# Performance work log

Hardware: AMD Instinct MI355X
Metric: run time of the kernel (lower is better)

## Reference

```python
import jax, jax.numpy as jnp
import numpy as np

N = 1048576   # total points across batch
C = 64        # in_planes
B = 16        # number of ragged segments (point clouds)
EPS = 1e-5


def setup_inputs() -> dict:
    key = jax.random.key(0)
    ks = jax.random.split(key, 4)
    x = jax.random.normal(ks[0], (N, C), dtype=jnp.float32)
    # cumulative end-offsets, strictly increasing, last == N
    rng = np.random.default_rng(0)
    w = rng.random(B) + 0.5
    ends = np.round(np.cumsum(w) / w.sum() * N).astype(np.int64)
    ends[-1] = N
    o = jnp.asarray(ends)
    # linear2: Linear(C, C) + ReLU (applied to per-segment mean)
    W2 = jax.random.normal(ks[1], (C, C), dtype=jnp.float32) / np.float32(np.sqrt(C))
    b2 = jnp.zeros((C,), jnp.float32)
    # linear1: BasicMLP(2C -> C): Linear + norm + ReLU
    W1 = jax.random.normal(ks[2], (2 * C, C), dtype=jnp.float32) / np.float32(np.sqrt(2 * C))
    b1 = jnp.zeros((C,), jnp.float32)
    gamma = jnp.ones((C,), jnp.float32)
    beta = jnp.zeros((C,), jnp.float32)
    return dict(x=x, o=o, W2=W2, b2=b2, W1=W1, b1=b1, gamma=gamma, beta=beta)


def reference(x, o, W2, b2, W1, b1, gamma, beta):
    n = x.shape[0]
    nseg = o.shape[0]
    # segment id of each point from cumulative offsets o
    seg = jnp.searchsorted(o, jnp.arange(n), side='right')          # [N]
    counts = jnp.diff(o, prepend=0).astype(x.dtype)                 # [B]
    # per-segment mean pool (x_b.sum(0) / cnt)
    sums = jax.ops.segment_sum(x, seg, num_segments=nseg)           # [B, C]
    means = sums / counts[:, None]
    # linear2: Linear + ReLU on the pooled vector
    xb = jax.nn.relu(means @ W2 + b2)                               # [B, C]
    # broadcast-repeat pooled feature back to points, concat with x
    h = jnp.concatenate([x, xb[seg]], axis=1)                       # [N, 2C]
    # linear1: Linear -> norm (LayerNorm stand-in for conditional norm) -> ReLU
    h = h @ W1 + b1                                                 # [N, C]
    mu = jnp.mean(h, axis=-1, keepdims=True)
    var = jnp.var(h, axis=-1, keepdims=True)
    h = (h - mu) * jax.lax.rsqrt(var + EPS) * gamma + beta
    return jax.nn.relu(h)
```

## Files before the change

kernel.cpp:

```cpp
#include <hip/hip_runtime.h>
#include <hip/hip_bf16.h>
#include <cstddef>

constexpr int C = 64;
constexpr int B = 16;

typedef __attribute__((ext_vector_type(8))) short bf16x8;
typedef __attribute__((ext_vector_type(4))) float f32x4;
typedef __attribute__((ext_vector_type(4))) unsigned int u32x4;

__device__ inline unsigned short f2bf(float f) {
    unsigned u = __builtin_bit_cast(unsigned, f);
    unsigned r = (u + 0x7FFFu + ((u >> 16) & 1u)) >> 16;
    return (unsigned short)r;
}

__device__ inline unsigned pk2(float a, float b) {
    __hip_bfloat162 t = __float22bfloat162_rn(float2{a, b});
    unsigned u;
    __builtin_memcpy(&u, &t, 4);
    return u;
}

__device__ inline bf16x8 cvt8(float4 u, float4 v) {
    u32x4 r;
    r[0] = pk2(u.x, u.y);
    r[1] = pk2(u.z, u.w);
    r[2] = pk2(v.x, v.y);
    r[3] = pk2(v.z, v.w);
    return __builtin_bit_cast(bf16x8, r);
}

__global__ __launch_bounds__(256) void seg_sum_kernel(
    const float* __restrict__ x, const int* __restrict__ o,
    float* __restrict__ sums, int N, int rows_per_block)
{
    __shared__ float lsum[B * C];
    const int tid = threadIdx.x;
    for (int i = tid; i < B * C; i += 256) lsum[i] = 0.0f;
    __syncthreads();

    const int c4 = (tid & 15) * 4;
    const int r0 = tid >> 4;
    const int row_begin = blockIdx.x * rows_per_block;
    const int row_end   = min(N, row_begin + rows_per_block);

    float ax = 0.f, ay = 0.f, az = 0.f, aw = 0.f;
    int seg = 0;
    int endcur = o[0];

    for (int r = row_begin + r0; r < row_end; r += 16) {
        while (r >= endcur) {
            if (ax != 0.f || ay != 0.f || az != 0.f || aw != 0.f) {
                atomicAdd(&lsum[seg * C + c4 + 0], ax);
                atomicAdd(&lsum[seg * C + c4 + 1], ay);
                atomicAdd(&lsum[seg * C + c4 + 2], az);
                atomicAdd(&lsum[seg * C + c4 + 3], aw);
                ax = ay = az = aw = 0.f;
            }
            ++seg;
            endcur = o[seg];
        }
        const float4 v = *reinterpret_cast<const float4*>(x + (size_t)r * C + c4);
        ax += v.x; ay += v.y; az += v.z; aw += v.w;
    }
    if (ax != 0.f || ay != 0.f || az != 0.f || aw != 0.f) {
        atomicAdd(&lsum[seg * C + c4 + 0], ax);
        atomicAdd(&lsum[seg * C + c4 + 1], ay);
        atomicAdd(&lsum[seg * C + c4 + 2], az);
        atomicAdd(&lsum[seg * C + c4 + 3], aw);
    }
    __syncthreads();

    for (int i = tid; i < B * C; i += 256) {
        const float v = lsum[i];
        if (v != 0.f) atomicAdd(&sums[i], v);
    }
}

__global__ __launch_bounds__(256) void main_mfma_kernel(
    const float* __restrict__ x, const int* __restrict__ o,
    const float* __restrict__ sums,
    const float* __restrict__ W2, const float* __restrict__ b2,
    const float* __restrict__ W1, const float* __restrict__ b1,
    const float* __restrict__ gamma, const float* __restrict__ beta,
    float* __restrict__ out, int N, int rows_per_wave)
{
    __shared__ float ms[B * C];
    __shared__ float xbs[B * C];
    __shared__ float vl[B * C];
    __shared__ unsigned short wbfs[4096];
    __shared__ int osh[B];

    const int tid = threadIdx.x;
    if (tid < B) osh[tid] = o[tid];
    __syncthreads();

    const int j = tid & 63;
    const int bq = tid >> 6;

#pragma unroll
    for (int q = 0; q < 4; ++q) {
        const int b = bq * 4 + q;
        const int cnt = osh[b] - (b ? osh[b - 1] : 0);
        ms[b * C + j] = sums[b * C + j] / (float)cnt;
    }
    __syncthreads();

    {
        float acc[4];
        const float bj = b2[j];
#pragma unroll
        for (int q = 0; q < 4; ++q) acc[q] = bj;
        for (int c = 0; c < C; ++c) {
            const float wv = W2[c * C + j];
#pragma unroll
            for (int q = 0; q < 4; ++q)
                acc[q] = fmaf(ms[(bq * 4 + q) * C + c], wv, acc[q]);
        }
#pragma unroll
        for (int q = 0; q < 4; ++q) xbs[(bq * 4 + q) * C + j] = fmaxf(acc[q], 0.f);
    }
    __syncthreads();

    {
        float acc[4];
        const float bj = b1[j];
#pragma unroll
        for (int q = 0; q < 4; ++q) acc[q] = bj;
        for (int jj = 0; jj < C; ++jj) {
            const float wv = W1[(C + jj) * C + j];
#pragma unroll
            for (int q = 0; q < 4; ++q)
                acc[q] = fmaf(xbs[(bq * 4 + q) * C + jj], wv, acc[q]);
        }
#pragma unroll
        for (int q = 0; q < 4; ++q) vl[(bq * 4 + q) * C + j] = acc[q];
    }

    for (int idx = tid; idx < 4096; idx += 256) {
        const int jj2 = idx & 7;
        const int ln  = (idx >> 3) & 63;
        const int tt  = (idx >> 9) & 1;
        const int ct  = idx >> 10;
        const int k   = tt * 32 + ((ln >> 4) * 8) + jj2;
        const int ch  = 4 * (ln & 15) + ct;
        wbfs[idx] = f2bf(W1[k * C + ch]);
    }
    __syncthreads();

    const int lane = tid & 63;
    const int wid  = tid >> 6;
    const int chb  = lane & 15;
    const int prow = (lane >> 4) * 4;

    bf16x8 wf[4][2];
#pragma unroll
    for (int ct = 0; ct < 4; ++ct)
#pragma unroll
        for (int t = 0; t < 2; ++t)
            wf[ct][t] = *reinterpret_cast<const bf16x8*>(wbfs + ((ct * 2 + t) * 64 + lane) * 8);

    const float4 g4  = *reinterpret_cast<const float4*>(gamma + 4 * chb);
    const float4 bt4 = *reinterpret_cast<const float4*>(beta  + 4 * chb);

    const int gw = blockIdx.x * 4 + wid;
    const int p_begin = gw * rows_per_wave;
    if (p_begin >= N) return;
    const int p_end = min(N, p_begin + rows_per_wave);

    int seg = 0;
    while (p_begin >= osh[seg]) ++seg;
    float4 vb = *reinterpret_cast<const float4*>(vl + seg * C + 4 * chb);

    for (int p0 = p_begin; p0 < p_end; p0 += 16) {
        const float* xr = x + (size_t)(p0 + chb) * C + ((lane >> 4) * 8);
        const float4 a0 = *reinterpret_cast<const float4*>(xr);
        const float4 a1 = *reinterpret_cast<const float4*>(xr + 4);
        const float4 a2 = *reinterpret_cast<const float4*>(xr + 32);
        const float4 a3 = *reinterpret_cast<const float4*>(xr + 36);
        const bf16x8 A0 = cvt8(a0, a1);
        const bf16x8 A1 = cvt8(a2, a3);

        f32x4 acc[4];
#pragma unroll
        for (int ct = 0; ct < 4; ++ct) {
            acc[ct] = f32x4{0.f, 0.f, 0.f, 0.f};
            acc[ct] = __builtin_amdgcn_mfma_f32_16x16x32_bf16(A0, wf[ct][0], acc[ct], 0, 0, 0);
            acc[ct] = __builtin_amdgcn_mfma_f32_16x16x32_bf16(A1, wf[ct][1], acc[ct], 0, 0, 0);
        }

        float h[4][4];
        if (p0 + 16 <= osh[seg]) {
#pragma unroll
            for (int r = 0; r < 4; ++r) {
                h[0][r] = acc[0][r] + vb.x;
                h[1][r] = acc[1][r] + vb.y;
                h[2][r] = acc[2][r] + vb.z;
                h[3][r] = acc[3][r] + vb.w;
            }
        } else {
#pragma unroll
            for (int r = 0; r < 4; ++r) {
                const int p = p0 + prow + r;
                int s = seg;
                while (p >= osh[s]) ++s;
                const float4 vbs = *reinterpret_cast<const float4*>(vl + s * C + 4 * chb);
                h[0][r] = acc[0][r] + vbs.x;
                h[1][r] = acc[1][r] + vbs.y;
                h[2][r] = acc[2][r] + vbs.z;
                h[3][r] = acc[3][r] + vbs.w;
            }
        }

#pragma unroll
        for (int r = 0; r < 4; ++r) {
            float s_ = (h[0][r] + h[1][r]) + (h[2][r] + h[3][r]);
            float q_ = fmaf(h[0][r], h[0][r],
                       fmaf(h[1][r], h[1][r],
                       fmaf(h[2][r], h[2][r], h[3][r] * h[3][r])));
#pragma unroll
            for (int m = 1; m < 16; m <<= 1) {
                s_ += __shfl_xor(s_, m, 64);
                q_ += __shfl_xor(q_, m, 64);
            }
            const float mean = s_ * (1.0f / 64.0f);
            const float var  = q_ * (1.0f / 64.0f) - mean * mean;
            const float rs   = rsqrtf(var + 1e-5f);
            const int p = p0 + prow + r;

            f32x4 y;
            y[0] = fmaxf((h[0][r] - mean) * rs * g4.x + bt4.x, 0.f);
            y[1] = fmaxf((h[1][r] - mean) * rs * g4.y + bt4.y, 0.f);
            y[2] = fmaxf((h[2][r] - mean) * rs * g4.z + bt4.z, 0.f);
            y[3] = fmaxf((h[3][r] - mean) * rs * g4.w + bt4.w, 0.f);
            __builtin_nontemporal_store(y, reinterpret_cast<f32x4*>(out + (size_t)p * C + 4 * chb));
        }

        const int pn = p0 + 16;
        if (pn < p_end && pn >= osh[seg]) {
            while (pn >= osh[seg]) ++seg;
            vb = *reinterpret_cast<const float4*>(vl + seg * C + 4 * chb);
        }
    }
}

extern "C" void kernel_launch(void* const* d_in, const int* in_sizes, int n_in,
                              void* d_out, int out_size, void* d_ws, size_t ws_size,
                              hipStream_t stream) {
    const float* x     = (const float*)d_in[0];
    const int*   o     = (const int*)d_in[1];
    const float* W2    = (const float*)d_in[2];
    const float* b2    = (const float*)d_in[3];
    const float* W1    = (const float*)d_in[4];
    const float* b1    = (const float*)d_in[5];
    const float* gamma = (const float*)d_in[6];
    const float* beta  = (const float*)d_in[7];
    float* out = (float*)d_out;

    const int N = in_sizes[0] / C;

    float* sums = (float*)d_ws;

    (void)hipMemsetAsync(sums, 0, B * C * sizeof(float), stream);

    const int rpb = 512;
    const int gridA = (N + rpb - 1) / rpb;
    seg_sum_kernel<<<gridA, 256, 0, stream>>>(x, o, sums, N, rpb);

    const int rpw = 128;
    const int nwaves = (N + rpw - 1) / rpw;
    const int gridC = (nwaves + 3) / 4;
    main_mfma_kernel<<<gridC, 256, 0, stream>>>(x, o, sums, W2, b2, W1, b1,
                                                gamma, beta, out, N, rpw);
}
```

Measured before the change: 152.7 us.

## Write bf16 copy of x in segment-sum pass and consume it in main kernel

The segment-sum pass now also converts x to bf16 and stores a half-size copy in workspace. The main MFMA kernel reads that copy instead of re-reading fp32 x and converting it. It also processes row chunks in reverse order, to reuse recently written data still in cache. Total DRAM bytes are roughly unchanged, because the extra write offsets the smaller read. The copy path depends on the workspace being large enough.

Measured after the change: 164.9 us. 8.0% more time.

```diff
diff --git a/kernel.cpp b/kernel.cpp
--- a/kernel.cpp
+++ b/kernel.cpp
@@ -31,45 +31,56 @@
     return __builtin_bit_cast(bf16x8, r);
 }
 
+__device__ inline f32x4 ntload4(const float* p) {
+    return __builtin_nontemporal_load(reinterpret_cast<const f32x4*>(p));
+}
+
+template<bool COPY>
 __global__ __launch_bounds__(256) void seg_sum_kernel(
     const float* __restrict__ x, const int* __restrict__ o,
-    float* __restrict__ sums, int N, int rows_per_block)
+    float* __restrict__ sums, unsigned short* __restrict__ xbf,
+    int N, int rows_per_block)
 {
     __shared__ float lsum[B * C];
     const int tid = threadIdx.x;
     for (int i = tid; i < B * C; i += 256) lsum[i] = 0.0f;
     __syncthreads();
 
-    const int c4 = (tid & 15) * 4;
-    const int r0 = tid >> 4;
+    const int c8 = (tid & 7) * 8;
+    const int r0 = tid >> 3;
     const int row_begin = blockIdx.x * rows_per_block;
     const int row_end   = min(N, row_begin + rows_per_block);
 
-    float ax = 0.f, ay = 0.f, az = 0.f, aw = 0.f;
+    float a[8];
+#pragma unroll
+    for (int i = 0; i < 8; ++i) a[i] = 0.f;
     int seg = 0;
     int endcur = o[0];
 
-    for (int r = row_begin + r0; r < row_end; r += 16) {
+    for (int r = row_begin + r0; r < row_end; r += 32) {
         while (r >= endcur) {
-            if (ax != 0.f || ay != 0.f || az != 0.f || aw != 0.f) {
-                atomicAdd(&lsum[seg * C + c4 + 0], ax);
-                atomicAdd(&lsum[seg * C + c4 + 1], ay);
-                atomicAdd(&lsum[seg * C + c4 + 2], az);
-                atomicAdd(&lsum[seg * C + c4 + 3], aw);
-                ax = ay = az = aw = 0.f;
-            }
+#pragma unroll
+            for (int i = 0; i < 8; ++i)
+                if (a[i] != 0.f) { atomicAdd(&lsum[seg * C + c8 + i], a[i]); a[i] = 0.f; }
             ++seg;
             endcur = o[seg];
         }
-        const float4 v = *reinterpret_cast<const float4*>(x + (size_t)r * C + c4);
-        ax += v.x; ay += v.y; az += v.z; aw += v.w;
-    }
-    if (ax != 0.f || ay != 0.f || az != 0.f || aw != 0.f) {
-        atomicAdd(&lsum[seg * C + c4 + 0], ax);
-        atomicAdd(&lsum[seg * C + c4 + 1], ay);
-        atomicAdd(&lsum[seg * C + c4 + 2], az);
-        atomicAdd(&lsum[seg * C + c4 + 3], aw);
-    }
+        const f32x4 v0 = ntload4(x + (size_t)r * C + c8);
+        const f32x4 v1 = ntload4(x + (size_t)r * C + c8 + 4);
+#pragma unroll
+        for (int i = 0; i < 4; ++i) { a[i] += v0[i]; a[4 + i] += v1[i]; }
+        if (COPY) {
+            u32x4 w;
+            w[0] = pk2(v0[0], v0[1]);
+            w[1] = pk2(v0[2], v0[3]);
+            w[2] = pk2(v1[0], v1[1]);
+            w[3] = pk2(v1[2], v1[3]);
+            *reinterpret_cast<u32x4*>(xbf + (size_t)r * C + c8) = w;
+        }
+    }
+#pragma unroll
+    for (int i = 0; i < 8; ++i)
+        if (a[i] != 0.f) atomicAdd(&lsum[seg * C + c8 + i], a[i]);
     __syncthreads();
 
     for (int i = tid; i < B * C; i += 256) {
@@ -78,13 +89,14 @@
     }
 }
 
+template<bool BF16>
 __global__ __launch_bounds__(256) void main_mfma_kernel(
-    const float* __restrict__ x, const int* __restrict__ o,
-    const float* __restrict__ sums,
+    const float* __restrict__ x, const unsigned short* __restrict__ xbf,
+    const int* __restrict__ o, const float* __restrict__ sums,
     const float* __restrict__ W2, const float* __restrict__ b2,
     const float* __restrict__ W1, const float* __restrict__ b1,
     const float* __restrict__ gamma, const float* __restrict__ beta,
-    float* __restrict__ out, int N, int rows_per_wave)
+    float* __restrict__ out, int N, int rows_per_wave, int ngw)
 {
     __shared__ float ms[B * C];
     __shared__ float xbs[B * C];
@@ -164,7 +176,9 @@
     const float4 g4  = *reinterpret_cast<const float4*>(gamma + 4 * chb);
     const float4 bt4 = *reinterpret_cast<const float4*>(beta  + 4 * chb);
 
-    const int gw = blockIdx.x * 4 + wid;
+    const int gw0 = blockIdx.x * 4 + wid;
+    if (gw0 >= ngw) return;
+    const int gw = ngw - 1 - gw0;
     const int p_begin = gw * rows_per_wave;
     if (p_begin >= N) return;
     const int p_end = min(N, p_begin + rows_per_wave);
@@ -174,13 +188,20 @@
     float4 vb = *reinterpret_cast<const float4*>(vl + seg * C + 4 * chb);
 
     for (int p0 = p_begin; p0 < p_end; p0 += 16) {
-        const float* xr = x + (size_t)(p0 + chb) * C + ((lane >> 4) * 8);
-        const float4 a0 = *reinterpret_cast<const float4*>(xr);
-        const float4 a1 = *reinterpret_cast<const float4*>(xr + 4);
-        const float4 a2 = *reinterpret_cast<const float4*>(xr + 32);
-        const float4 a3 = *reinterpret_cast<const float4*>(xr + 36);
-        const bf16x8 A0 = cvt8(a0, a1);
-        const bf16x8 A1 = cvt8(a2, a3);
+        bf16x8 A0, A1;
+        if constexpr (BF16) {
+            const unsigned short* xr = xbf + (size_t)(p0 + chb) * C + ((lane >> 4) * 8);
+            A0 = *reinterpret_cast<const bf16x8*>(xr);
+            A1 = *reinterpret_cast<const bf16x8*>(xr + 32);
+        } else {
+            const float* xr = x + (size_t)(p0 + chb) * C + ((lane >> 4) * 8);
+            const float4 a0 = *reinterpret_cast<const float4*>(xr);
+            const float4 a1 = *reinterpret_cast<const float4*>(xr + 4);
+            const float4 a2 = *reinterpret_cast<const float4*>(xr + 32);
+            const float4 a3 = *reinterpret_cast<const float4*>(xr + 36);
+            A0 = cvt8(a0, a1);
+            A1 = cvt8(a2, a3);
+        }
 
         f32x4 acc[4];
 #pragma unroll
@@ -261,16 +282,25 @@
     const int N = in_sizes[0] / C;
 
     float* sums = (float*)d_ws;
+    unsigned short* xbf = (unsigned short*)((char*)d_ws + 4096);
+    const size_t need = 4096 + (size_t)N * C * sizeof(unsigned short);
+    const bool use_copy = ws_size >= need;
 
     (void)hipMemsetAsync(sums, 0, B * C * sizeof(float), stream);
 
     const int rpb = 512;
     const int gridA = (N + rpb - 1) / rpb;
-    seg_sum_kernel<<<gridA, 256, 0, stream>>>(x, o, sums, N, rpb);
-
     const int rpw = 128;
-    const int nwaves = (N + rpw - 1) / rpw;
-    const int gridC = (nwaves + 3) / 4;
-    main_mfma_kernel<<<gridC, 256, 0, stream>>>(x, o, sums, W2, b2, W1, b1,
-                                                gamma, beta, out, N, rpw);
-}
+    const int ngw = (N + rpw - 1) / rpw;
+    const int gridC = (ngw + 3) / 4;
+
+    if (use_copy) {
+        seg_sum_kernel<true><<<gridA, 256, 0, stream>>>(x, o, sums, xbf, N, rpb);
+        main_mfma_kernel<true><<<gridC, 256, 0, stream>>>(x, xbf, o, sums, W2, b2, W1, b1,
+                                                          gamma, beta, out, N, rpw, ngw);
+    } else {
+        seg_sum_kernel<false><<<gridA, 256, 0, stream>>>(x, o, sums, xbf, N, rpb);
+        main_mfma_kernel<false><<<gridC, 256, 0, stream>>>(x, xbf, o, sums, W2, b2, W1, b1,
+                                                           gamma, beta, out, N, rpw, ngw);
+    }
+}
```
